# Optimization experiments

Hardware: AMD Instinct MI355X
Metric: run time of the kernel (lower is better)

Reference implementation:

```python
import jax, jax.numpy as jnp
import numpy as np

B, L, D, H = 2, 2048, 2048, 16
HD = D // H  # 128, must be even for RoPE


def rope(x, seq_len, theta=10000.0):
    """Apply RoPE to x of shape [B, H, L, Dh]."""
    d = x.shape[-1]
    freqs = 1.0 / theta ** (jnp.arange(0, d, 2, dtype=x.dtype) / d)  # [d/2]
    t = jnp.arange(seq_len, dtype=x.dtype)
    f = jnp.outer(t, freqs)                      # [L, d/2]
    sin = jnp.repeat(jnp.sin(f), 2, axis=-1)     # [L, d]
    cos = jnp.repeat(jnp.cos(f), 2, axis=-1)
    x1, x2 = x[..., ::2], x[..., 1::2]
    x_rot = jnp.stack([-x2, x1], axis=-1).reshape(x.shape)
    return x * cos + x_rot * sin


def setup_inputs() -> dict:
    key = jax.random.key(0)
    k1, k2, k3 = jax.random.split(key, 3)
    x = jax.random.normal(k1, (B, L, D), dtype=jnp.float32)
    w_qkv = jax.random.normal(k2, (D, 3 * D), dtype=jnp.float32) * (1.0 / np.sqrt(D))
    w_proj = jax.random.normal(k3, (D, D), dtype=jnp.float32) * (1.0 / np.sqrt(D))
    return {"x": x, "w_qkv": w_qkv, "w_proj": w_proj}


def reference(x, w_qkv, w_proj):
    Bc, Lc, Dc = x.shape
    scale = 1.0 / np.sqrt(HD)
    qkv = (x @ w_qkv).reshape(Bc, Lc, 3, H, HD)
    q, k, v = qkv[:, :, 0], qkv[:, :, 1], qkv[:, :, 2]   # [B, L, H, Dh]
    # transpose to [B, H, L, Dh], then RoPE (position axis = L)
    q = rope(jnp.transpose(q, (0, 2, 1, 3)), Lc)
    k = rope(jnp.transpose(k, (0, 2, 1, 3)), Lc)
    v = jnp.transpose(v, (0, 2, 1, 3))
    att = jnp.einsum("bhqd,bhkd->bhqk", q, k) * scale   # [B, H, L, L]
    att = jax.nn.softmax(att, axis=-1)
    out = jnp.einsum("bhqk,bhkd->bhqd", att, v)          # [B, H, L, Dh]
    out = jnp.transpose(out, (0, 2, 1, 3)).reshape(Bc, Lc, Dc)
    return out @ w_proj
```

## Files before the change

### kernel.cpp

```cpp
#include <hip/hip_runtime.h>
#include <hip/hip_bf16.h>
#include <cstdint>

typedef short short8 __attribute__((ext_vector_type(8)));
typedef float f32x4 __attribute__((ext_vector_type(4)));
typedef float f32x16 __attribute__((ext_vector_type(16)));
typedef int i32x4 __attribute__((ext_vector_type(4)));

#define AS1 __attribute__((address_space(1)))
#define AS3 __attribute__((address_space(3)))

static __device__ __forceinline__ void async_cp16(const void* g, void* l) {
  __builtin_amdgcn_global_load_lds((const AS1 unsigned int*)g, (AS3 unsigned int*)l, 16, 0, 0);
}

static __device__ __forceinline__ ushort f2bf(float f) {
  unsigned u = __builtin_bit_cast(unsigned, f);
  u += 0x7fffu + ((u >> 16) & 1u);
  return (ushort)(u >> 16);
}
static __device__ __forceinline__ float bf2f(ushort h) {
  unsigned u = ((unsigned)h) << 16;
  return __builtin_bit_cast(float, u);
}

#define FENCE asm volatile("" ::: "memory")
#define BARRIER do { FENCE; __builtin_amdgcn_s_barrier(); FENCE; } while (0)
#define WAITLGKM asm volatile("s_waitcnt lgkmcnt(0)" ::: "memory")
#define WAITVM(N) asm volatile("s_waitcnt vmcnt(" #N ")" ::: "memory")

__global__ void cvt_bf16_kernel(const float* __restrict__ in, ushort* __restrict__ out, int n4) {
  int i = blockIdx.x * blockDim.x + threadIdx.x;
  if (i >= n4) return;
  float4 v = ((const float4*)in)[i];
  ushort4 o;
  o.x = f2bf(v.x); o.y = f2bf(v.y); o.z = f2bf(v.z); o.w = f2bf(v.w);
  ((ushort4*)out)[i] = o;
}

__global__ void transpose_cvt_kernel(const float* __restrict__ in, ushort* __restrict__ out,
                                     int R, int C) {
  __shared__ ushort tile[32][33];
  int c0 = blockIdx.x * 32, r0 = blockIdx.y * 32;
  int tx = threadIdx.x, ty = threadIdx.y;
  for (int j = 0; j < 32; j += 8)
    tile[ty + j][tx] = f2bf(in[(size_t)(r0 + ty + j) * C + c0 + tx]);
  __syncthreads();
  for (int j = 0; j < 32; j += 8)
    out[(size_t)(c0 + ty + j) * R + r0 + tx] = tile[tx][ty + j];
}

__global__ void rope_tab_kernel(float2* __restrict__ tab) {
  int idx = blockIdx.x * 256 + threadIdx.x;
  int i = idx & 63, l = idx >> 6;
  float inv = __builtin_amdgcn_exp2f(-(float)i * (13.287712379549449f / 64.0f));
  float f = (float)l * inv;
  float s, c;
  sincosf(f, &s, &c);
  tab[idx] = make_float2(c, s);
}

__global__ __launch_bounds__(512, 2) void gemm_qkv_kernel(
    const ushort* __restrict__ A, const ushort* __restrict__ Bt,
    ushort* __restrict__ qr, ushort* __restrict__ kr, ushort* __restrict__ vt,
    const float2* __restrict__ rtab, int K, int N) {
  __shared__ __align__(16) ushort smem[65536];
  const int tid = threadIdx.x;
  const int wave = tid >> 6, lane = tid & 63;
  const int wm = wave >> 2, wn = wave & 3;
  const int m0 = blockIdx.y * 256, n0 = blockIdx.x * 256;
  const int frl = lane & 15, fq = lane >> 4;
  const int sx = fq ^ (frl & 7);
  const int srow = tid >> 3;
  const int slog8 = (((tid & 7) ^ ((tid >> 3) & 7)) << 3);

  const ushort* aG = A + (size_t)(m0 + srow) * K + slog8;
  const ushort* bG = Bt + (size_t)(n0 + srow) * K + slog8;
  ushort* lw = smem + wave * 512;

  f32x4 acc[8][4] = {};
  short8 aF[4][2], bF[2][2][2];

  auto stA = [&](int tt, int h) {
    ushort* l = lw + (tt & 1) * 32768 + h * 8192;
    const ushort* g = aG + (size_t)(h * 128) * K + tt * 64;
    async_cp16(g, l);
    async_cp16(g + (size_t)64 * K, l + 4096);
  };
  auto stB = [&](int tt, int h) {
    ushort* l = lw + (tt & 1) * 32768 + 16384 + h * 8192;
    const ushort* g = bG + (size_t)(h * 128) * K + tt * 64;
    async_cp16(g, l);
    async_cp16(g + (size_t)64 * K, l + 4096);
  };
  auto LDA = [&](int buf, int mh) {
#pragma unroll
    for (int mf = 0; mf < 4; ++mf)
#pragma unroll
      for (int kk = 0; kk < 2; ++kk)
        aF[mf][kk] = *(const short8*)(smem + buf * 32768 +
            (wm * 128 + mh * 64 + mf * 16 + frl) * 64 + ((sx ^ (kk << 2)) << 3));
  };
  auto LDB = [&](int buf, int nh) {
#pragma unroll
    for (int j = 0; j < 2; ++j)
#pragma unroll
      for (int kk = 0; kk < 2; ++kk)
        bF[nh][j][kk] = *(const short8*)(smem + buf * 32768 + 16384 +
            (wn * 64 + nh * 32 + j * 16 + frl) * 64 + ((sx ^ (kk << 2)) << 3));
  };
  auto MFMAQ = [&](int mh, int nh) {
    __builtin_amdgcn_s_setprio(1);
#pragma unroll
    for (int mf = 0; mf < 4; ++mf)
#pragma unroll
      for (int j = 0; j < 2; ++j)
#pragma unroll
        for (int kk = 0; kk < 2; ++kk)
          acc[mh * 4 + mf][nh * 2 + j] = __builtin_amdgcn_mfma_f32_16x16x32_bf16(
              aF[mf][kk], bF[nh][j][kk], acc[mh * 4 + mf][nh * 2 + j], 0, 0, 0);
    __builtin_amdgcn_s_setprio(0);
  };

  stB(0, 0); stB(0, 1); stA(0, 0); stA(0, 1);
  stB(1, 0); stB(1, 1);
  WAITVM(4);
  BARRIER;

  const int NT = K >> 6;
  for (int i = 0; i < NT / 2 - 1; ++i) {
    const int t = 2 * i;
    LDA(0, 0); LDB(0, 0); stA(t + 1, 0);
    BARRIER; WAITLGKM; MFMAQ(0, 0); BARRIER;
    LDB(0, 1); stA(t + 1, 1);
    BARRIER; WAITLGKM; MFMAQ(0, 1); BARRIER;
    LDA(0, 1); stB(t + 2, 0);
    BARRIER; WAITLGKM; MFMAQ(1, 0); BARRIER;
    stB(t + 2, 1);
    BARRIER; WAITLGKM; MFMAQ(1, 1); WAITVM(4); BARRIER;
    LDA(1, 0); LDB(1, 0); stA(t + 2, 0);
    BARRIER; WAITLGKM; MFMAQ(0, 0); BARRIER;
    LDB(1, 1); stA(t + 2, 1);
    BARRIER; WAITLGKM; MFMAQ(0, 1); BARRIER;
    LDA(1, 1); stB(t + 3, 0);
    BARRIER; WAITLGKM; MFMAQ(1, 0); BARRIER;
    stB(t + 3, 1);
    BARRIER; WAITLGKM; MFMAQ(1, 1); WAITVM(4); BARRIER;
  }
  {
    const int t = NT - 2;
    LDA(0, 0); LDB(0, 0); stA(t + 1, 0);
    BARRIER; WAITLGKM; MFMAQ(0, 0); BARRIER;
    LDB(0, 1); stA(t + 1, 1);
    BARRIER; WAITLGKM; MFMAQ(0, 1); BARRIER;
    LDA(0, 1);
    BARRIER; WAITLGKM; MFMAQ(1, 0); BARRIER;
    BARRIER; WAITLGKM; MFMAQ(1, 1); WAITVM(0); BARRIER;
    LDA(1, 0); LDB(1, 0);
    BARRIER; WAITLGKM; MFMAQ(0, 0); BARRIER;
    LDB(1, 1);
    BARRIER; WAITLGKM; MFMAQ(0, 1); BARRIER;
    LDA(1, 1);
    BARRIER; WAITLGKM; MFMAQ(1, 0); BARRIER;
    BARRIER; WAITLGKM; MFMAQ(1, 1); BARRIER;
  }

  const int rq = fq * 4;
  if (n0 < 4096) {
    ushort* dst = (n0 >= 2048) ? kr : qr;
#pragma unroll
    for (int mi = 0; mi < 8; ++mi)
#pragma unroll
      for (int ni = 0; ni < 4; ++ni) {
        int col = n0 + wn * 64 + ni * 16 + frl;
        int rem = col & 2047, h = rem >> 7, dh = rem & 127;
        int ip = dh >> 1;
        float sgn = (dh & 1) ? 1.0f : -1.0f;
#pragma unroll
        for (int r = 0; r < 4; ++r) {
          int row = m0 + wm * 128 + mi * 16 + rq + r;
          int b = row >> 11, l = row & 2047;
          float v = acc[mi][ni][r];
          float vp = __shfl_xor(v, 1);
          float2 cs2 = rtab[l * 64 + ip];
          float o = v * cs2.x + sgn * vp * cs2.y;
          dst[((size_t)((b << 4) + h) * 2048 + l) * 128 + dh] = f2bf(o);
        }
      }
  } else {
    ushort* vtile = smem + wave * 1024;
    const int col0 = n0 + wn * 64;
    const int row0 = m0 + wm * 128;
    const int b = row0 >> 11, l0 = row0 & 2047;
    const int swz = (frl & 3) << 4;
#pragma unroll
    for (int hm = 0; hm < 2; ++hm)
#pragma unroll
      for (int ni = 0; ni < 4; ++ni) {
#pragma unroll
        for (int mi = 0; mi < 4; ++mi)
#pragma unroll
          for (int r = 0; r < 4; ++r) {
            int ll = mi * 16 + rq + r;
            vtile[frl * 64 + (ll ^ swz)] = f2bf(acc[hm * 4 + mi][ni][r]);
          }
#pragma unroll
        for (int tt = 0; tt < 2; ++tt) {
          int dl = tt * 8 + (lane >> 3);
          int l8 = (lane & 7) * 8;
          int lsw = l8 ^ ((dl & 3) << 4);
          int rem = (col0 + ni * 16 + dl) & 2047;
          int h = rem >> 7, dh = rem & 127;
          *(short8*)(vt + ((size_t)((b << 4) + h) * 128 + dh) * 2048 + l0 + hm * 64 + l8) =
              *(const short8*)(vtile + dl * 64 + lsw);
        }
      }
  }
}

__global__ __launch_bounds__(256) void gemm_out_kernel(
    const ushort* __restrict__ A, const ushort* __restrict__ Bt,
    float* __restrict__ C, int K, int N) {
  __shared__ __align__(16) ushort As[128 * 32];
  __shared__ __align__(16) ushort Bs[128 * 32];
  const int tid = threadIdx.x;
  const int wave = tid >> 6, lane = tid & 63;
  const int wr = (wave >> 1) * 64, wc = (wave & 1) * 64;
  const int m0 = blockIdx.y * 128, n0 = blockIdx.x * 128;
  const int l4 = lane >> 2, lb8 = (lane & 3) * 8;
  const int fr = lane & 15, fq8 = (lane >> 4) * 8;

  f32x4 acc[4][4] = {};

  for (int k0 = 0; k0 < K; k0 += 32) {
#pragma unroll
    for (int j = 0; j < 2; ++j) {
      const int r = wave * 32 + j * 16 + l4;
      async_cp16(A + (size_t)(m0 + r) * K + k0 + lb8, As + wave * 1024 + j * 512);
      async_cp16(Bt + (size_t)(n0 + r) * K + k0 + lb8, Bs + wave * 1024 + j * 512);
    }
    __syncthreads();
    short8 af[4], bf_[4];
#pragma unroll
    for (int i = 0; i < 4; ++i) {
      af[i] = *(const short8*)(As + (wr + i * 16 + fr) * 32 + fq8);
      bf_[i] = *(const short8*)(Bs + (wc + i * 16 + fr) * 32 + fq8);
    }
#pragma unroll
    for (int mi = 0; mi < 4; ++mi)
#pragma unroll
      for (int ni = 0; ni < 4; ++ni)
        acc[mi][ni] = __builtin_amdgcn_mfma_f32_16x16x32_bf16(af[mi], bf_[ni], acc[mi][ni], 0, 0, 0);
    __syncthreads();
  }

  const int rq = (lane >> 4) * 4;
#pragma unroll
  for (int mi = 0; mi < 4; ++mi)
#pragma unroll
    for (int ni = 0; ni < 4; ++ni) {
      int col = n0 + wc + ni * 16 + fr;
#pragma unroll
      for (int r = 0; r < 4; ++r) {
        int row = m0 + wr + mi * 16 + rq + r;
        C[(size_t)row * N + col] = acc[mi][ni][r];
      }
    }
}

__global__ __launch_bounds__(512, 2) void flash_kernel(
    const ushort* __restrict__ qr, const ushort* __restrict__ kr,
    const ushort* __restrict__ vtg, ushort* __restrict__ att) {
  __shared__ __align__(16) ushort KV[2][16384];

  const int tid = threadIdx.x;
  const int wave = tid >> 6, lane = tid & 63;
  const int bid = blockIdx.x;
  const int swzb = (bid & 7) * 32 + (bid >> 3);
  const int qt = swzb & 7;
  const int bh = swzb >> 3;
  const int q0 = qt * 256 + wave * 32;
  const size_t bh_base = (size_t)bh * 2048 * 128;

  const int qi = lane & 31, hi = lane >> 5;
  const float cs = 0.08838834764831845f * 1.4426950408889634f;
  const int rsw = (qi & 7) << 3;

  const int krow0 = wave * 8 + (lane >> 4);
  const int kgc = (lane & 15) * 8;
  const int vrow0 = wave * 16 + (lane >> 3);
  const int vgc = (lane & 7) * 8;

  auto stage = [&](int kt, int buf) {
#pragma unroll
    for (int i = 0; i < 2; ++i) {
      const int krow = krow0 + i * 4;
      async_cp16(kr + bh_base + (size_t)(kt * 64 + krow) * 128 + (kgc ^ ((krow & 7) << 3)),
                 &KV[buf][(wave * 2 + i) * 512]);
      const int vrow = vrow0 + i * 8;
      async_cp16(vtg + bh_base + (size_t)vrow * 2048 + kt * 64 + (vgc ^ ((vrow & 7) << 3)),
                 &KV[buf][8192 + (wave * 2 + i) * 512]);
    }
  };

  short8 qf[8];
  {
    const ushort* qp = qr + bh_base + (size_t)(q0 + qi) * 128 + hi * 8;
#pragma unroll
    for (int c = 0; c < 8; ++c) qf[c] = *(const short8*)(qp + c * 16);
  }

  f32x16 oacc[4];
#pragma unroll
  for (int nt = 0; nt < 4; ++nt)
#pragma unroll
    for (int r = 0; r < 16; ++r) oacc[nt][r] = 0.f;
  float l_lane = 0.f;

  stage(0, 0);
  stage(1, 1);
  WAITVM(4);
  BARRIER;

#pragma unroll 2
  for (int kt = 0; kt < 32; ++kt) {
    const int bo = (kt & 1) * 16384;
    const ushort* kv = &KV[0][0];

    f32x16 s0, s1;
#pragma unroll
    for (int r = 0; r < 16; ++r) { s0[r] = 0.f; s1[r] = 0.f; }
    const ushort* kp0 = kv + bo + (size_t)(0 * 32 + qi) * 128;
    const ushort* kp1 = kv + bo + (size_t)(1 * 32 + qi) * 128;
    __builtin_amdgcn_s_setprio(1);
#pragma unroll
    for (int c = 0; c < 8; ++c) {
      const int co = (c * 16 + hi * 8) ^ rsw;
      short8 kf0 = *(const short8*)(kp0 + co);
      short8 kf1 = *(const short8*)(kp1 + co);
      s0 = __builtin_amdgcn_mfma_f32_32x32x16_bf16(kf0, qf[c], s0, 0, 0, 0);
      s1 = __builtin_amdgcn_mfma_f32_32x32x16_bf16(kf1, qf[c], s1, 0, 0, 0);
    }
    __builtin_amdgcn_s_setprio(0);

    int pk[2][8];
#pragma unroll
    for (int m = 0; m < 8; ++m) {
      float a0 = __builtin_amdgcn_exp2f(s0[2 * m] * cs);
      float a1 = __builtin_amdgcn_exp2f(s0[2 * m + 1] * cs);
      float b0 = __builtin_amdgcn_exp2f(s1[2 * m] * cs);
      float b1 = __builtin_amdgcn_exp2f(s1[2 * m + 1] * cs);
      l_lane += (a0 + a1) + (b0 + b1);
      pk[0][m] = (int)f2bf(a0) | ((int)f2bf(a1) << 16);
      pk[1][m] = (int)f2bf(b0) | ((int)f2bf(b1) << 16);
    }

    __builtin_amdgcn_s_setprio(1);
#pragma unroll
    for (int ks = 0; ks < 4; ++ks) {
      const int kb = ks >> 1, s2 = ks & 1;
      const int a0 = pk[kb][4 * s2 + 0], a1 = pk[kb][4 * s2 + 1];
      const int a2 = pk[kb][4 * s2 + 2], a3 = pk[kb][4 * s2 + 3];
      const int p0 = __shfl_xor(a0, 32), p1 = __shfl_xor(a1, 32);
      const int p2 = __shfl_xor(a2, 32), p3 = __shfl_xor(a3, 32);
      i32x4 w;
      w[0] = hi ? p2 : a0;
      w[1] = hi ? p3 : a1;
      w[2] = hi ? a2 : p0;
      w[3] = hi ? a3 : p1;
      short8 pa = __builtin_bit_cast(short8, w);
      const int vco = (ks * 16 + hi * 8) ^ rsw;
#pragma unroll
      for (int nt = 0; nt < 4; ++nt) {
        short8 vf = *(const short8*)(kv + bo + 8192 + (size_t)(nt * 32 + qi) * 64 + vco);
        oacc[nt] = __builtin_amdgcn_mfma_f32_32x32x16_bf16(pa, vf, oacc[nt], 0, 0, 0);
      }
    }
    __builtin_amdgcn_s_setprio(0);

    BARRIER;
    if (kt < 30) {
      stage(kt + 2, kt & 1);
      WAITVM(4);
    } else {
      WAITVM(0);
    }
    BARRIER;
  }

  l_lane += __shfl_xor(l_lane, 32);
  const float linv = 1.0f / l_lane;
  const int b = bh >> 4, h = bh & 15;
#pragma unroll
  for (int r = 0; r < 16; ++r) {
    const int crow = (r & 3) + 8 * (r >> 2) + 4 * hi;
    const float inv = __shfl(linv, crow);
    const size_t rowa = (size_t)(b * 2048 + q0 + crow) * 2048 + h * 128;
#pragma unroll
    for (int nt = 0; nt < 4; ++nt)
      att[rowa + nt * 32 + qi] = f2bf(oacc[nt][r] * inv);
  }
}

extern "C" void kernel_launch(void* const* d_in, const int* in_sizes, int n_in,
                              void* d_out, int out_size, void* d_ws, size_t ws_size,
                              hipStream_t stream) {
  const float* x = (const float*)d_in[0];
  const float* w_qkv = (const float*)d_in[1];
  const float* w_proj = (const float*)d_in[2];
  float* out = (float*)d_out;

  char* p = (char*)d_ws;
  ushort* xb = (ushort*)p;  p += (size_t)4096 * 2048 * 2;
  ushort* wqt = (ushort*)p; p += (size_t)6144 * 2048 * 2;
  ushort* wpt = (ushort*)p; p += (size_t)2048 * 2048 * 2;
  ushort* qr = (ushort*)p;  p += (size_t)32 * 2048 * 128 * 2;
  ushort* kr = (ushort*)p;  p += (size_t)32 * 2048 * 128 * 2;
  ushort* vt = (ushort*)p;  p += (size_t)32 * 2048 * 128 * 2;
  ushort* att = (ushort*)p; p += (size_t)4096 * 2048 * 2;
  float2* rtab = (float2*)p; p += (size_t)2048 * 64 * 8;

  rope_tab_kernel<<<512, 256, 0, stream>>>(rtab);
  cvt_bf16_kernel<<<8192, 256, 0, stream>>>(x, xb, 4096 * 2048 / 4);
  transpose_cvt_kernel<<<dim3(192, 64), dim3(32, 8), 0, stream>>>(w_qkv, wqt, 2048, 6144);
  transpose_cvt_kernel<<<dim3(64, 64), dim3(32, 8), 0, stream>>>(w_proj, wpt, 2048, 2048);
  gemm_qkv_kernel<<<dim3(24, 16), 512, 0, stream>>>(xb, wqt, qr, kr, vt, rtab, 2048, 6144);
  flash_kernel<<<256, 512, 0, stream>>>(qr, kr, vt, att);
  gemm_out_kernel<<<dim3(16, 32), 256, 0, stream>>>(att, wpt, out, 2048, 2048);
}
```

Before: 403.5 us.

## Rewrite output projection GEMM with double-buffered 128x256 tiles and interleaved loads

The output projection GEMM changes from a 128x128 tile with a single LDS buffer and a sync every 32-wide K step to a 128x256 tile with 8 waves and BK=64. It double-buffers swizzled LDS tiles and interleaves async global-to-LDS loads with MFMA quarters under raised wave priority. The aim is to hide memory latency, cut LDS bank conflicts and reduce barrier stalls in a kernel that was fully serialized. In exchange it uses far more LDS, places many barriers per iteration, and halves the grid to 256 blocks, which may underfill the GPU.

```diff
diff --git a/kernel.cpp b/kernel.cpp
--- a/kernel.cpp
+++ b/kernel.cpp
@@ -218,52 +218,120 @@
   }
 }
 
-__global__ __launch_bounds__(256) void gemm_out_kernel(
+__global__ __launch_bounds__(512, 2) void gemm_out_kernel(
     const ushort* __restrict__ A, const ushort* __restrict__ Bt,
     float* __restrict__ C, int K, int N) {
-  __shared__ __align__(16) ushort As[128 * 32];
-  __shared__ __align__(16) ushort Bs[128 * 32];
+  __shared__ __align__(16) ushort smem[49152];
   const int tid = threadIdx.x;
   const int wave = tid >> 6, lane = tid & 63;
-  const int wr = (wave >> 1) * 64, wc = (wave & 1) * 64;
-  const int m0 = blockIdx.y * 128, n0 = blockIdx.x * 128;
-  const int l4 = lane >> 2, lb8 = (lane & 3) * 8;
-  const int fr = lane & 15, fq8 = (lane >> 4) * 8;
+  const int wm = wave >> 2, wn = wave & 3;
+  const int m0 = blockIdx.y * 128, n0 = blockIdx.x * 256;
+  const int frl = lane & 15, fq = lane >> 4;
+  const int sx = fq ^ (frl & 7);
+  const int srow = tid >> 3;
+  const int slog8 = (((tid & 7) ^ ((tid >> 3) & 7)) << 3);
+
+  const ushort* aG = A + (size_t)(m0 + srow) * K + slog8;
+  const ushort* bG = Bt + (size_t)(n0 + srow) * K + slog8;
+  ushort* lw = smem + wave * 512;
 
   f32x4 acc[4][4] = {};
-
-  for (int k0 = 0; k0 < K; k0 += 32) {
-#pragma unroll
-    for (int j = 0; j < 2; ++j) {
-      const int r = wave * 32 + j * 16 + l4;
-      async_cp16(A + (size_t)(m0 + r) * K + k0 + lb8, As + wave * 1024 + j * 512);
-      async_cp16(Bt + (size_t)(n0 + r) * K + k0 + lb8, Bs + wave * 1024 + j * 512);
-    }
-    __syncthreads();
-    short8 af[4], bf_[4];
-#pragma unroll
-    for (int i = 0; i < 4; ++i) {
-      af[i] = *(const short8*)(As + (wr + i * 16 + fr) * 32 + fq8);
-      bf_[i] = *(const short8*)(Bs + (wc + i * 16 + fr) * 32 + fq8);
-    }
-#pragma unroll
-    for (int mi = 0; mi < 4; ++mi)
-#pragma unroll
-      for (int ni = 0; ni < 4; ++ni)
-        acc[mi][ni] = __builtin_amdgcn_mfma_f32_16x16x32_bf16(af[mi], bf_[ni], acc[mi][ni], 0, 0, 0);
-    __syncthreads();
-  }
-
-  const int rq = (lane >> 4) * 4;
+  short8 aF[2][2], bF[2][2][2];
+
+  auto stA = [&](int tt) {
+    ushort* l = lw + (tt & 1) * 24576;
+    const ushort* g = aG + tt * 64;
+    async_cp16(g, l);
+    async_cp16(g + (size_t)64 * K, l + 4096);
+  };
+  auto stB = [&](int tt, int h) {
+    ushort* l = lw + (tt & 1) * 24576 + 8192 + h * 8192;
+    const ushort* g = bG + (size_t)(h * 128) * K + tt * 64;
+    async_cp16(g, l);
+    async_cp16(g + (size_t)64 * K, l + 4096);
+  };
+  auto LDA = [&](int buf, int mh) {
+#pragma unroll
+    for (int mf = 0; mf < 2; ++mf)
+#pragma unroll
+      for (int kk = 0; kk < 2; ++kk)
+        aF[mf][kk] = *(const short8*)(smem + buf * 24576 +
+            (wm * 64 + mh * 32 + mf * 16 + frl) * 64 + ((sx ^ (kk << 2)) << 3));
+  };
+  auto LDB = [&](int buf, int nh) {
+#pragma unroll
+    for (int j = 0; j < 2; ++j)
+#pragma unroll
+      for (int kk = 0; kk < 2; ++kk)
+        bF[nh][j][kk] = *(const short8*)(smem + buf * 24576 + 8192 +
+            (wn * 64 + nh * 32 + j * 16 + frl) * 64 + ((sx ^ (kk << 2)) << 3));
+  };
+  auto MFMAQ = [&](int mh, int nh) {
+    __builtin_amdgcn_s_setprio(1);
+#pragma unroll
+    for (int mf = 0; mf < 2; ++mf)
+#pragma unroll
+      for (int j = 0; j < 2; ++j)
+#pragma unroll
+        for (int kk = 0; kk < 2; ++kk)
+          acc[mh * 2 + mf][nh * 2 + j] = __builtin_amdgcn_mfma_f32_16x16x32_bf16(
+              aF[mf][kk], bF[nh][j][kk], acc[mh * 2 + mf][nh * 2 + j], 0, 0, 0);
+    __builtin_amdgcn_s_setprio(0);
+  };
+
+  stB(0, 0); stB(0, 1); stA(0);
+  stB(1, 0); stB(1, 1);
+  WAITVM(4);
+  BARRIER;
+
+  const int NT = K >> 6;
+  for (int i = 0; i < NT / 2 - 1; ++i) {
+    const int t = 2 * i;
+    LDA(0, 0); LDB(0, 0); stA(t + 1);
+    BARRIER; WAITLGKM; MFMAQ(0, 0); BARRIER;
+    LDB(0, 1);
+    BARRIER; WAITLGKM; MFMAQ(0, 1); BARRIER;
+    LDA(0, 1); stB(t + 2, 0);
+    BARRIER; WAITLGKM; MFMAQ(1, 0); BARRIER;
+    stB(t + 2, 1);
+    BARRIER; WAITLGKM; MFMAQ(1, 1); WAITVM(4); BARRIER;
+    LDA(1, 0); LDB(1, 0); stA(t + 2);
+    BARRIER; WAITLGKM; MFMAQ(0, 0); BARRIER;
+    LDB(1, 1);
+    BARRIER; WAITLGKM; MFMAQ(0, 1); BARRIER;
+    LDA(1, 1); stB(t + 3, 0);
+    BARRIER; WAITLGKM; MFMAQ(1, 0); BARRIER;
+    stB(t + 3, 1);
+    BARRIER; WAITLGKM; MFMAQ(1, 1); WAITVM(4); BARRIER;
+  }
+  {
+    const int t = NT - 2;
+    LDA(0, 0); LDB(0, 0); stA(t + 1);
+    BARRIER; WAITLGKM; MFMAQ(0, 0); BARRIER;
+    LDB(0, 1);
+    BARRIER; WAITLGKM; MFMAQ(0, 1); BARRIER;
+    LDA(0, 1);
+    BARRIER; WAITLGKM; MFMAQ(1, 0); BARRIER;
+    BARRIER; WAITLGKM; MFMAQ(1, 1); WAITVM(0); BARRIER;
+    LDA(1, 0); LDB(1, 0);
+    BARRIER; WAITLGKM; MFMAQ(0, 0); BARRIER;
+    LDB(1, 1);
+    BARRIER; WAITLGKM; MFMAQ(0, 1); BARRIER;
+    LDA(1, 1);
+    BARRIER; WAITLGKM; MFMAQ(1, 0); BARRIER;
+    BARRIER; WAITLGKM; MFMAQ(1, 1); BARRIER;
+  }
+
+  const int rq = fq * 4;
 #pragma unroll
   for (int mi = 0; mi < 4; ++mi)
 #pragma unroll
-    for (int ni = 0; ni < 4; ++ni) {
-      int col = n0 + wc + ni * 16 + fr;
+    for (int nj = 0; nj < 4; ++nj) {
+      int col = n0 + wn * 64 + nj * 16 + frl;
 #pragma unroll
       for (int r = 0; r < 4; ++r) {
-        int row = m0 + wr + mi * 16 + rq + r;
-        C[(size_t)row * N + col] = acc[mi][ni][r];
+        int row = m0 + wm * 64 + mi * 16 + rq + r;
+        C[(size_t)row * N + col] = acc[mi][nj][r];
       }
     }
 }
@@ -426,5 +494,5 @@
   transpose_cvt_kernel<<<dim3(64, 64), dim3(32, 8), 0, stream>>>(w_proj, wpt, 2048, 2048);
   gemm_qkv_kernel<<<dim3(24, 16), 512, 0, stream>>>(xb, wqt, qr, kr, vt, rtab, 2048, 6144);
   flash_kernel<<<256, 512, 0, stream>>>(qr, kr, vt, att);
-  gemm_out_kernel<<<dim3(16, 32), 256, 0, stream>>>(att, wpt, out, 2048, 2048);
-}
+  gemm_out_kernel<<<dim3(8, 32), 512, 0, stream>>>(att, wpt, out, 2048, 2048);
+}
```

Result: faster. 391.8 us (-2.9%).
